# Performance work log

Measured on AMD Instinct MI355X. Metric: run time of the kernel, lower is better.

Reference implementation:

```python
import jax, jax.numpy as jnp
import numpy as np

TEXT_DIM = 1024
FEAT_DIM = 1024
NUM_HEADS = 16
HEAD_DIM = FEAT_DIM // NUM_HEADS
EPS = 1e-6


def rms_norm(x, w):
    # LlamaRMSNorm: compute in fp32, scale by learned weight
    xf = x.astype(jnp.float32)
    var = jnp.mean(xf * xf, axis=-1, keepdims=True)
    return (xf * jax.lax.rsqrt(var + EPS)).astype(x.dtype) * w


def setup_inputs() -> dict:
    key = jax.random.key(0)
    ks = jax.random.split(key, 8)
    def xavier(k, shape, gain=1.0):
        fan_in, fan_out = shape[1], shape[0]
        lim = gain * np.sqrt(6.0 / (fan_in + fan_out))
        return jax.random.uniform(k, shape, jnp.float32, -lim, lim)
    return {
        "text": jax.random.normal(ks[0], (8, 512, TEXT_DIM), jnp.float32),
        "features": jax.random.normal(ks[1], (8, 1024, FEAT_DIM), jnp.float32),
        "W_q": xavier(ks[2], (FEAT_DIM, TEXT_DIM)),
        "b_q": jnp.zeros((FEAT_DIM,), jnp.float32),
        "W_k": xavier(ks[3], (FEAT_DIM, FEAT_DIM)),
        "b_k": jnp.zeros((FEAT_DIM,), jnp.float32),
        "W_o": xavier(ks[4], (FEAT_DIM, FEAT_DIM), gain=0.1),
        "b_o": jnp.zeros((FEAT_DIM,), jnp.float32),
        "g_feat": jnp.ones((FEAT_DIM,), jnp.float32),
        "g_q": jnp.ones((FEAT_DIM,), jnp.float32),
        "g_k": jnp.ones((FEAT_DIM,), jnp.float32),
    }


def reference(text, features, W_q, b_q, W_k, b_k, W_o, b_o, g_feat, g_q, g_k):
    B, T, _ = text.shape
    _, N, _ = features.shape
    feats = rms_norm(features, g_feat)                      # [B,N,Df]
    Q = rms_norm(text @ W_q.T + b_q, g_q)                   # [B,T,Df]
    K = rms_norm(feats @ W_k.T + b_k, g_k)                  # [B,N,Df]
    Qh = Q.reshape(B, T, NUM_HEADS, HEAD_DIM)
    Kh = K.reshape(B, N, NUM_HEADS, HEAD_DIM)
    Vh = feats.reshape(B, N, NUM_HEADS, HEAD_DIM)
    scores = jnp.einsum("bthd,bnhd->bhtn", Qh, Kh) / np.sqrt(HEAD_DIM).astype(np.float32)
    attn = jax.nn.softmax(scores, axis=-1)                  # [B,H,T,N]
    out = jnp.einsum("bhtn,bnhd->bthd", attn, Vh).reshape(B, T, FEAT_DIM)
    return out @ W_o.T + b_o
```

## Files before the change

### kernel.cpp

```cpp
#include <hip/hip_runtime.h>
#include <hip/hip_bf16.h>


typedef unsigned short u16;
typedef __bf16 bf16x8 __attribute__((ext_vector_type(8)));
typedef float f32x4 __attribute__((ext_vector_type(4)));

__device__ inline f32x4 mfma16(bf16x8 a, bf16x8 b, f32x4 c) {
    return __builtin_amdgcn_mfma_f32_16x16x32_bf16(a, b, c, 0, 0, 0);
}

__device__ inline u16 f2bf(float f) {
    union { float f; unsigned u; } v; v.f = f;
    unsigned r = v.u + 0x7fffu + ((v.u >> 16) & 1u);
    return (u16)(r >> 16);
}

__device__ inline float bf2f(u16 x) {
    union { unsigned u; float f; } v; v.u = ((unsigned)x) << 16; return v.f;
}

__device__ inline unsigned pk_bf16(float a, float b) {
    union { float f; unsigned u; } x, y; x.f = a; y.f = b;
    return __builtin_amdgcn_perm(y.u + 0x8000u, x.u + 0x8000u, 0x07060302u);
}

__device__ inline void load_lds16(const void* g, void* l) {
    __builtin_amdgcn_global_load_lds(
        (const __attribute__((address_space(1))) void*)g,
        (__attribute__((address_space(3))) void*)l, 16, 0, 0);
}

__global__ __launch_bounds__(256) void cast_rows_kernel(const float* __restrict__ text,
                                                        const float* __restrict__ Wq,
                                                        const float* __restrict__ Wk,
                                                        const float* __restrict__ Wo,
                                                        const float* __restrict__ features,
                                                        u16* __restrict__ otext, u16* __restrict__ oWq,
                                                        u16* __restrict__ oWk, u16* __restrict__ oWo,
                                                        float* __restrict__ ssbuf) {
    int blk = blockIdx.x, tid = threadIdx.x;
    if (blk < 7168) {
        int i = blk * 256 + tid;
        const float* src; u16* dst; int off;
        if (i < 1048576)      { src = text; dst = otext; off = i; }
        else if (i < 1310720) { src = Wq;   dst = oWq;   off = i - 1048576; }
        else if (i < 1572864) { src = Wk;   dst = oWk;   off = i - 1310720; }
        else                  { src = Wo;   dst = oWo;   off = i - 1572864; }
        float4 v = ((const float4*)src)[off];
        uint2 p; p.x = pk_bf16(v.x, v.y); p.y = pk_bf16(v.z, v.w);
        ((uint2*)dst)[off] = p;
    } else {
        int row = (blk - 7168) * 4 + (tid >> 6);
        int lane = tid & 63;
        const float4* rp = (const float4*)(features + (size_t)row * 1024) + lane * 4;
        float ss = 0.0f;
        #pragma unroll
        for (int i = 0; i < 4; ++i) {
            float4 v = rp[i];
            ss += v.x * v.x + v.y * v.y + v.z * v.z + v.w * v.w;
        }
        #pragma unroll
        for (int m = 1; m < 64; m <<= 1) ss += __shfl_xor(ss, m, 64);
        if (lane == 0) ssbuf[row] = ss;
    }
}

__global__ __launch_bounds__(256) void normT_kernel(const float* __restrict__ features,
                                                    const float* __restrict__ ssbuf,
                                                    const float* __restrict__ g,
                                                    u16* __restrict__ feats_bf,
                                                    u16* __restrict__ Vt) {
    __shared__ __align__(16) u16 tile[64][72];
    int tid = threadIdx.x, b = blockIdx.z;
    int n0 = blockIdx.x * 64, d0 = blockIdx.y * 64;
    int r = tid >> 2, cs = (tid & 3) * 16;
    int grow = b * 1024 + n0 + r;

    float rs = rsqrtf(ssbuf[grow] * (1.0f / 1024.0f) + 1e-6f);
    const float4* src = (const float4*)(features + (size_t)grow * 1024 + d0 + cs);
    const float4* gp  = (const float4*)(g + d0 + cs);
    union { u16 s[16]; uint4 v[2]; } ob;
    #pragma unroll
    for (int i = 0; i < 4; ++i) {
        float4 v = src[i], gv = gp[i];
        unsigned lo = pk_bf16(v.x * rs * gv.x, v.y * rs * gv.y);
        unsigned hi = pk_bf16(v.z * rs * gv.z, v.w * rs * gv.w);
        ((unsigned*)ob.s)[i * 2]     = lo;
        ((unsigned*)ob.s)[i * 2 + 1] = hi;
    }
    uint4* dst = (uint4*)(feats_bf + (size_t)grow * 1024 + d0 + cs);
    dst[0] = ob.v[0]; dst[1] = ob.v[1];
    #pragma unroll
    for (int i = 0; i < 16; ++i) tile[r][cs + i] = ob.s[i];
    __syncthreads();
    union { u16 s[8]; uint4 v; } t0, t1;
    #pragma unroll
    for (int i = 0; i < 8; ++i) { t0.s[i] = tile[cs + i][r]; t1.s[i] = tile[cs + 8 + i][r]; }
    u16* tdst = Vt + ((size_t)(b * 1024 + d0 + r)) * 1024 + n0 + cs;
    *(uint4*)tdst = t0.v;
    *(uint4*)(tdst + 8) = t1.v;
}

__global__ __launch_bounds__(256) void rmsnorm_qk_kernel(u16* __restrict__ QK,
                                                         const float* __restrict__ g_q,
                                                         const float* __restrict__ g_k,
                                                         float qscale) {
    int tid = threadIdx.x;
    int row = blockIdx.x * 4 + (tid >> 6);
    int lane = tid & 63;
    const float* g = (row < 4096) ? g_q : g_k;
    float outsc = (row < 4096) ? qscale : 1.0f;

    u16* rp = QK + (size_t)row * 1024 + lane * 16;
    union { u16 s[16]; uint4 v[2]; } in;
    in.v[0] = *(const uint4*)rp;
    in.v[1] = *(const uint4*)(rp + 8);
    float x[16], ss = 0.0f;
    #pragma unroll
    for (int i = 0; i < 16; ++i) { x[i] = bf2f(in.s[i]); ss += x[i] * x[i]; }
    #pragma unroll
    for (int m = 1; m < 64; m <<= 1) ss += __shfl_xor(ss, m, 64);
    float rs = rsqrtf(ss * (1.0f / 1024.0f) + 1e-6f) * outsc;
    const float4* gp = (const float4*)(g + lane * 16);
    union { unsigned u[8]; uint4 v[2]; } ob;
    #pragma unroll
    for (int i = 0; i < 4; ++i) {
        float4 gv = gp[i];
        ob.u[i * 2]     = pk_bf16(x[i * 4 + 0] * rs * gv.x, x[i * 4 + 1] * rs * gv.y);
        ob.u[i * 2 + 1] = pk_bf16(x[i * 4 + 2] * rs * gv.z, x[i * 4 + 3] * rs * gv.w);
    }
    *(uint4*)rp = ob.v[0];
    *(uint4*)(rp + 8) = ob.v[1];
}

template <bool BF16OUT>
__device__ __forceinline__ void gemm64_bk64(const u16* __restrict__ A, const u16* __restrict__ B,
                                            const float* __restrict__ bias, void* __restrict__ Cout,
                                            int m_blk, int n_blk, int K, int N,
                                            u16* As, u16* Bs) {
    int tid = threadIdx.x, wave = tid >> 6, lane = tid & 63;
    int quad = lane >> 4, l15 = lane & 15;
    int wm = wave & 1, wn = wave >> 1;
    int arow = tid >> 2, ac = (tid & 3) * 8;

    f32x4 acc[4][2] = {};

    for (int k0 = 0; k0 < K; k0 += 64) {
        #pragma unroll
        for (int kh = 0; kh < 2; ++kh)
            #pragma unroll
            for (int rh = 0; rh < 2; ++rh)
                load_lds16(A + (size_t)(m_blk + rh * 64 + arow) * K + k0 + kh * 32 + ac,
                           As + kh * 4096 + rh * 2048 + (wave * 64) * 8);
        #pragma unroll
        for (int kh = 0; kh < 2; ++kh)
            load_lds16(B + (size_t)(n_blk + arow) * K + k0 + kh * 32 + ac,
                       Bs + kh * 2048 + (wave * 64) * 8);
        __syncthreads();
        #pragma unroll
        for (int kh = 0; kh < 2; ++kh) {
            bf16x8 af[4], bfr[2];
            #pragma unroll
            for (int t = 0; t < 4; ++t)
                af[t] = *(const bf16x8*)&As[kh * 4096 + (wm * 64 + t * 16 + l15) * 32 + quad * 8];
            #pragma unroll
            for (int t = 0; t < 2; ++t)
                bfr[t] = *(const bf16x8*)&Bs[kh * 2048 + (wn * 32 + t * 16 + l15) * 32 + quad * 8];
            #pragma unroll
            for (int mt = 0; mt < 4; ++mt)
                #pragma unroll
                for (int nt = 0; nt < 2; ++nt)
                    acc[mt][nt] = mfma16(af[mt], bfr[nt], acc[mt][nt]);
        }
        __syncthreads();
    }
    #pragma unroll
    for (int nt = 0; nt < 2; ++nt) {
        int col = n_blk + wn * 32 + nt * 16 + l15;
        float bv = bias[col];
        #pragma unroll
        for (int mt = 0; mt < 4; ++mt) {
            int row0 = m_blk + wm * 64 + mt * 16 + quad * 4;
            #pragma unroll
            for (int r = 0; r < 4; ++r) {
                float val = acc[mt][nt][r] + bv;
                if (BF16OUT) ((u16*)Cout)[(size_t)(row0 + r) * N + col] = f2bf(val);
                else       ((float*)Cout)[(size_t)(row0 + r) * N + col] = val;
            }
        }
    }
}

__global__ __launch_bounds__(256) void gemm_qk_kernel(const u16* __restrict__ text_bf,
                                                      const u16* __restrict__ Wq,
                                                      const u16* __restrict__ feats_bf,
                                                      const u16* __restrict__ Wk,
                                                      const float* __restrict__ b_q,
                                                      const float* __restrict__ b_k,
                                                      u16* __restrict__ QK) {
    __shared__ __align__(16) u16 As[2 * 128 * 32];
    __shared__ __align__(16) u16 Bs[2 * 64 * 32];
    int id = blockIdx.x;
    if (id < 512) {
        gemm64_bk64<true>(text_bf, Wq, b_q, QK, (id & 31) * 128, (id >> 5) * 64, 1024, 1024, As, Bs);
    } else {
        id -= 512;
        gemm64_bk64<true>(feats_bf, Wk, b_k, QK + 4096 * 1024,
                          (id & 63) * 128, (id >> 6) * 64, 1024, 1024, As, Bs);
    }
}

__global__ __launch_bounds__(256) void gemm_o_kernel(const u16* __restrict__ A,
                                                     const u16* __restrict__ B,
                                                     const float* __restrict__ bias,
                                                     float* __restrict__ C) {
    __shared__ __align__(16) u16 As[2 * 128 * 32];
    __shared__ __align__(16) u16 Bs[2 * 64 * 32];
    int id = blockIdx.x;
    gemm64_bk64<false>(A, B, bias, C, (id & 31) * 128, (id >> 5) * 64, 1024, 1024, As, Bs);
}

__global__ __launch_bounds__(256) void attn_kernel(const u16* __restrict__ Q,
                                                   const u16* __restrict__ K,
                                                   const u16* __restrict__ Vt,
                                                   u16* __restrict__ Out) {
    int bh = blockIdx.x, qt = blockIdx.y;
    int b = bh >> 4, h = bh & 15;
    int tid = threadIdx.x, wave = tid >> 6, lane = tid & 63;
    int quad = lane >> 4, l15 = lane & 15;

    __shared__ __align__(16) u16 Ks[64 * 64];
    __shared__ __align__(16) u16 Vs[64 * 64];
    __shared__ __align__(16) u16 Plds[4][16 * 72];
    u16* Pw = &Plds[wave][0];

    const size_t qoff = ((size_t)(b * 512 + qt * 64 + wave * 16 + l15)) * 1024 + h * 64 + quad * 8;
    bf16x8 qf0 = *(const bf16x8*)(Q + qoff);
    bf16x8 qf1 = *(const bf16x8*)(Q + qoff + 32);

    int srl = lane >> 3, scl = lane & 7;
    const u16* Kbase = K + ((size_t)(b * 1024)) * 1024 + h * 64;
    const u16* Vbase = Vt + ((size_t)(b * 1024 + h * 64)) * 1024;

    __bf16 onev = (__bf16)1.0f;
    bf16x8 ones = {onev, onev, onev, onev, onev, onev, onev, onev};

    f32x4 o[4] = {};
    f32x4 lac = {0.0f, 0.0f, 0.0f, 0.0f};

    for (int n0 = 0; n0 < 1024; n0 += 64) {
        #pragma unroll
        for (int j = 0; j < 2; ++j) {
            int row = wave * 16 + j * 8 + srl;
            load_lds16(Kbase + (size_t)(n0 + row) * 1024 + (scl ^ srl) * 8,
                       Ks + (wave * 16 + j * 8) * 64);
            load_lds16(Vbase + (size_t)row * 1024 + n0 + (scl ^ srl) * 8,
                       Vs + (wave * 16 + j * 8) * 64);
        }
        __syncthreads();

        f32x4 s[4];
        #pragma unroll
        for (int nt = 0; nt < 4; ++nt) {
            int R = nt * 16 + l15;
            int c1 = (quad ^ (l15 & 7)) * 8;
            bf16x8 kf0 = *(const bf16x8*)&Ks[R * 64 + c1];
            bf16x8 kf1 = *(const bf16x8*)&Ks[R * 64 + (c1 ^ 32)];
            f32x4 z = {-16.0f, -16.0f, -16.0f, -16.0f};
            s[nt] = mfma16(kf0, qf0, z);
            s[nt] = mfma16(kf1, qf1, s[nt]);
        }

        #pragma unroll
        for (int nt = 0; nt < 4; ++nt) {
            uint2 pk;
            pk.x = pk_bf16(exp2f(s[nt][0]), exp2f(s[nt][1]));
            pk.y = pk_bf16(exp2f(s[nt][2]), exp2f(s[nt][3]));
            *(uint2*)&Pw[l15 * 72 + nt * 16 + quad * 4] = pk;
        }

        bf16x8 pf[2];
        #pragma unroll
        for (int kc = 0; kc < 2; ++kc)
            pf[kc] = *(const bf16x8*)&Pw[l15 * 72 + kc * 32 + quad * 8];
        #pragma unroll
        for (int kc = 0; kc < 2; ++kc) {
            lac = mfma16(ones, pf[kc], lac);
            #pragma unroll
            for (int dt = 0; dt < 4; ++dt) {
                int d = dt * 16 + l15;
                int ch = ((kc * 4 + quad) ^ (l15 & 7)) * 8;
                bf16x8 vf = *(const bf16x8*)&Vs[d * 64 + ch];
                o[dt] = mfma16(vf, pf[kc], o[dt]);
            }
        }
        __syncthreads();
    }

    float il = 1.0f / lac[0];
    size_t obase = ((size_t)(b * 512 + qt * 64 + wave * 16 + l15)) * 1024 + h * 64 + quad * 4;
    #pragma unroll
    for (int dt = 0; dt < 4; ++dt) {
        uint2 pk;
        pk.x = pk_bf16(o[dt][0] * il, o[dt][1] * il);
        pk.y = pk_bf16(o[dt][2] * il, o[dt][3] * il);
        *(uint2*)(Out + obase + dt * 16) = pk;
    }
}

extern "C" void kernel_launch(void* const* d_in, const int* in_sizes, int n_in,
                              void* d_out, int out_size, void* d_ws, size_t ws_size,
                              hipStream_t stream) {
    const float* text     = (const float*)d_in[0];
    const float* features = (const float*)d_in[1];
    const float* W_q      = (const float*)d_in[2];
    const float* b_q      = (const float*)d_in[3];
    const float* W_k      = (const float*)d_in[4];
    const float* b_k      = (const float*)d_in[5];
    const float* W_o      = (const float*)d_in[6];
    const float* b_o      = (const float*)d_in[7];
    const float* g_feat   = (const float*)d_in[8];
    const float* g_q      = (const float*)d_in[9];
    const float* g_k      = (const float*)d_in[10];

    char* ws = (char*)d_ws;
    u16*   text_bf  = (u16*)(ws + 0);
    u16*   Wq_bf    = (u16*)(ws + 8388608);
    u16*   Wk_bf    = (u16*)(ws + 10485760);
    u16*   Wo_bf    = (u16*)(ws + 12582912);
    u16*   feats_bf = (u16*)(ws + 14680064);
    u16*   Vt       = (u16*)(ws + 31457280);
    u16*   QKbuf    = (u16*)(ws + 48234496);
    u16*   attn_bf  = (u16*)(ws + 73400320);
    float* ssbuf    = (float*)(ws + 81788928);

    const float QSCALE = 0.18033688011112042f;

    cast_rows_kernel<<<9216, 256, 0, stream>>>(text, W_q, W_k, W_o, features,
                                               text_bf, Wq_bf, Wk_bf, Wo_bf, ssbuf);
    normT_kernel<<<dim3(16, 16, 8), 256, 0, stream>>>(features, ssbuf, g_feat, feats_bf, Vt);
    gemm_qk_kernel<<<1536, 256, 0, stream>>>(text_bf, Wq_bf, feats_bf, Wk_bf, b_q, b_k, QKbuf);
    rmsnorm_qk_kernel<<<3072, 256, 0, stream>>>(QKbuf, g_q, g_k, QSCALE);
    attn_kernel<<<dim3(128, 8), 256, 0, stream>>>(QKbuf, QKbuf + 4096 * 1024, Vt, attn_bf);
    gemm_o_kernel<<<512, 256, 0, stream>>>(attn_bf, Wo_bf, b_o, (float*)d_out);
}
```

Measured before the change: 225.0 us.

## Split attention key range across waves with 128-key tiles and LDS reduction

The attention kernel now gives each wave a 32-key slice of a 128-key tile and all 64 query rows, instead of each wave owning 16 query rows over 64-key tiles. The partial outputs and row sums from the four waves are combined at the end through a shared-memory tree reduction. The aim is to halve the number of K/V tile loads and barriers, and to reuse each K and V fragment read from LDS across four query tiles. In exchange the kernel holds many more accumulator registers (launch bounds set to 2 blocks) and pays extra reduction and barrier cost at the end. The softmax still relies on a fixed offset instead of a running max, unchanged from before.

```diff
diff --git a/kernel.cpp b/kernel.cpp
--- a/kernel.cpp
+++ b/kernel.cpp
@@ -84,10 +84,8 @@
     #pragma unroll
     for (int i = 0; i < 4; ++i) {
         float4 v = src[i], gv = gp[i];
-        unsigned lo = pk_bf16(v.x * rs * gv.x, v.y * rs * gv.y);
-        unsigned hi = pk_bf16(v.z * rs * gv.z, v.w * rs * gv.w);
-        ((unsigned*)ob.s)[i * 2]     = lo;
-        ((unsigned*)ob.s)[i * 2 + 1] = hi;
+        ((unsigned*)ob.s)[i * 2]     = pk_bf16(v.x * rs * gv.x, v.y * rs * gv.y);
+        ((unsigned*)ob.s)[i * 2 + 1] = pk_bf16(v.z * rs * gv.z, v.w * rs * gv.w);
     }
     uint4* dst = (uint4*)(feats_bf + (size_t)grow * 1024 + d0 + cs);
     dst[0] = ob.v[0]; dst[1] = ob.v[1];
@@ -221,91 +219,148 @@
     gemm64_bk64<false>(A, B, bias, C, (id & 31) * 128, (id >> 5) * 64, 1024, 1024, As, Bs);
 }
 
-__global__ __launch_bounds__(256) void attn_kernel(const u16* __restrict__ Q,
-                                                   const u16* __restrict__ K,
-                                                   const u16* __restrict__ Vt,
-                                                   u16* __restrict__ Out) {
+__global__ __launch_bounds__(256, 2) void attn_kernel(const u16* __restrict__ Q,
+                                                      const u16* __restrict__ K,
+                                                      const u16* __restrict__ Vt,
+                                                      u16* __restrict__ Out) {
     int bh = blockIdx.x, qt = blockIdx.y;
     int b = bh >> 4, h = bh & 15;
     int tid = threadIdx.x, wave = tid >> 6, lane = tid & 63;
     int quad = lane >> 4, l15 = lane & 15;
 
-    __shared__ __align__(16) u16 Ks[64 * 64];
-    __shared__ __align__(16) u16 Vs[64 * 64];
-    __shared__ __align__(16) u16 Plds[4][16 * 72];
-    u16* Pw = &Plds[wave][0];
-
-    const size_t qoff = ((size_t)(b * 512 + qt * 64 + wave * 16 + l15)) * 1024 + h * 64 + quad * 8;
-    bf16x8 qf0 = *(const bf16x8*)(Q + qoff);
-    bf16x8 qf1 = *(const bf16x8*)(Q + qoff + 32);
-
-    int srl = lane >> 3, scl = lane & 7;
+    __shared__ __align__(16) char smem[49152];
+    u16* Ks = (u16*)smem;
+    u16* Vs = (u16*)(smem + 16384);
+    u16* Pw = (u16*)(smem + 32768) + wave * 2048;
+
+    const u16* Qbase = Q + ((size_t)(b * 512 + qt * 64)) * 1024 + h * 64;
+    bf16x8 qf[4][2];
+    #pragma unroll
+    for (int mt = 0; mt < 4; ++mt)
+        #pragma unroll
+        for (int kh = 0; kh < 2; ++kh)
+            qf[mt][kh] = *(const bf16x8*)(Qbase + (size_t)(mt * 16 + l15) * 1024 + kh * 32 + quad * 8);
+
+    int krl = lane >> 3, kcl = lane & 7;
+    int vrl = lane >> 4, vcl = lane & 15;
     const u16* Kbase = K + ((size_t)(b * 1024)) * 1024 + h * 64;
     const u16* Vbase = Vt + ((size_t)(b * 1024 + h * 64)) * 1024;
 
     __bf16 onev = (__bf16)1.0f;
     bf16x8 ones = {onev, onev, onev, onev, onev, onev, onev, onev};
 
-    f32x4 o[4] = {};
-    f32x4 lac = {0.0f, 0.0f, 0.0f, 0.0f};
-
-    for (int n0 = 0; n0 < 1024; n0 += 64) {
-        #pragma unroll
-        for (int j = 0; j < 2; ++j) {
-            int row = wave * 16 + j * 8 + srl;
-            load_lds16(Kbase + (size_t)(n0 + row) * 1024 + (scl ^ srl) * 8,
-                       Ks + (wave * 16 + j * 8) * 64);
-            load_lds16(Vbase + (size_t)row * 1024 + n0 + (scl ^ srl) * 8,
-                       Vs + (wave * 16 + j * 8) * 64);
+    f32x4 o[4][4] = {};
+    f32x4 lac[4] = {};
+
+    for (int n0 = 0; n0 < 1024; n0 += 128) {
+        #pragma unroll
+        for (int j = 0; j < 4; ++j) {
+            int krow = wave * 32 + j * 8 + krl;
+            load_lds16(Kbase + (size_t)(n0 + krow) * 1024 + (kcl ^ (krow & 7)) * 8,
+                       Ks + (wave * 32 + j * 8) * 64);
+            int vrow = wave * 16 + j * 4 + vrl;
+            load_lds16(Vbase + (size_t)vrow * 1024 + n0 + (vcl ^ (vrow & 7)) * 8,
+                       Vs + (wave * 16 + j * 4) * 128);
         }
         __syncthreads();
 
-        f32x4 s[4];
-        #pragma unroll
-        for (int nt = 0; nt < 4; ++nt) {
-            int R = nt * 16 + l15;
-            int c1 = (quad ^ (l15 & 7)) * 8;
-            bf16x8 kf0 = *(const bf16x8*)&Ks[R * 64 + c1];
-            bf16x8 kf1 = *(const bf16x8*)&Ks[R * 64 + (c1 ^ 32)];
-            f32x4 z = {-16.0f, -16.0f, -16.0f, -16.0f};
-            s[nt] = mfma16(kf0, qf0, z);
-            s[nt] = mfma16(kf1, qf1, s[nt]);
-        }
-
-        #pragma unroll
-        for (int nt = 0; nt < 4; ++nt) {
-            uint2 pk;
-            pk.x = pk_bf16(exp2f(s[nt][0]), exp2f(s[nt][1]));
-            pk.y = pk_bf16(exp2f(s[nt][2]), exp2f(s[nt][3]));
-            *(uint2*)&Pw[l15 * 72 + nt * 16 + quad * 4] = pk;
-        }
-
-        bf16x8 pf[2];
-        #pragma unroll
-        for (int kc = 0; kc < 2; ++kc)
-            pf[kc] = *(const bf16x8*)&Pw[l15 * 72 + kc * 32 + quad * 8];
-        #pragma unroll
-        for (int kc = 0; kc < 2; ++kc) {
-            lac = mfma16(ones, pf[kc], lac);
+        int ns = wave * 32;
+
+        #pragma unroll
+        for (int nt = 0; nt < 2; ++nt) {
+            int R = ns + nt * 16 + l15;
+            bf16x8 kf0 = *(const bf16x8*)&Ks[R * 64 + ((quad) ^ (l15 & 7)) * 8];
+            bf16x8 kf1 = *(const bf16x8*)&Ks[R * 64 + ((4 + quad) ^ (l15 & 7)) * 8];
+            #pragma unroll
+            for (int mt = 0; mt < 4; ++mt) {
+                f32x4 z = {-16.0f, -16.0f, -16.0f, -16.0f};
+                f32x4 s = mfma16(kf0, qf[mt][0], z);
+                s = mfma16(kf1, qf[mt][1], s);
+                uint2 pk;
+                pk.x = pk_bf16(exp2f(s[0]), exp2f(s[1]));
+                pk.y = pk_bf16(exp2f(s[2]), exp2f(s[3]));
+                int cp = (nt * 2 + (quad >> 1)) ^ (l15 & 3);
+                *(uint2*)&Pw[(mt * 16 + l15) * 32 + cp * 8 + (quad & 1) * 4] = pk;
+            }
+        }
+
+        bf16x8 pf[4];
+        #pragma unroll
+        for (int mt = 0; mt < 4; ++mt)
+            pf[mt] = *(const bf16x8*)&Pw[(mt * 16 + l15) * 32 + (quad ^ (l15 & 3)) * 8];
+        #pragma unroll
+        for (int dt = 0; dt < 4; ++dt) {
+            int d = dt * 16 + l15;
+            bf16x8 vf = *(const bf16x8*)&Vs[d * 128 + ((wave * 4 + quad) ^ (l15 & 7)) * 8];
+            #pragma unroll
+            for (int mt = 0; mt < 4; ++mt)
+                o[dt][mt] = mfma16(vf, pf[mt], o[dt][mt]);
+        }
+        #pragma unroll
+        for (int mt = 0; mt < 4; ++mt)
+            lac[mt] = mfma16(ones, pf[mt], lac[mt]);
+        __syncthreads();
+    }
+
+    float* rbuf0 = (float*)smem;
+    float* rbuf1 = (float*)(smem + 17408);
+    float* lbuf0 = (float*)(smem + 34816);
+    float* lbuf1 = (float*)(smem + 35072);
+
+    if (wave >= 2) {
+        float* rb = (wave == 2) ? rbuf0 : rbuf1;
+        float* lb = (wave == 2) ? lbuf0 : lbuf1;
+        #pragma unroll
+        for (int dt = 0; dt < 4; ++dt)
+            #pragma unroll
+            for (int mt = 0; mt < 4; ++mt)
+                *(f32x4*)&rb[(mt * 16 + l15) * 68 + dt * 16 + quad * 4] = o[dt][mt];
+        if (quad == 0)
+            #pragma unroll
+            for (int mt = 0; mt < 4; ++mt) lb[mt * 16 + l15] = lac[mt][0];
+    }
+    __syncthreads();
+    if (wave < 2) {
+        float* rb = (wave == 0) ? rbuf0 : rbuf1;
+        float* lb = (wave == 0) ? lbuf0 : lbuf1;
+        #pragma unroll
+        for (int dt = 0; dt < 4; ++dt)
+            #pragma unroll
+            for (int mt = 0; mt < 4; ++mt)
+                o[dt][mt] += *(const f32x4*)&rb[(mt * 16 + l15) * 68 + dt * 16 + quad * 4];
+        #pragma unroll
+        for (int mt = 0; mt < 4; ++mt) lac[mt][0] += lb[mt * 16 + l15];
+    }
+    __syncthreads();
+    if (wave == 1) {
+        #pragma unroll
+        for (int dt = 0; dt < 4; ++dt)
+            #pragma unroll
+            for (int mt = 0; mt < 4; ++mt)
+                *(f32x4*)&rbuf1[(mt * 16 + l15) * 68 + dt * 16 + quad * 4] = o[dt][mt];
+        if (quad == 0)
+            #pragma unroll
+            for (int mt = 0; mt < 4; ++mt) lbuf1[mt * 16 + l15] = lac[mt][0];
+    }
+    __syncthreads();
+    if (wave == 0) {
+        #pragma unroll
+        for (int dt = 0; dt < 4; ++dt)
+            #pragma unroll
+            for (int mt = 0; mt < 4; ++mt)
+                o[dt][mt] += *(const f32x4*)&rbuf1[(mt * 16 + l15) * 68 + dt * 16 + quad * 4];
+        #pragma unroll
+        for (int mt = 0; mt < 4; ++mt) {
+            float il = 1.0f / (lac[mt][0] + lbuf1[mt * 16 + l15]);
+            size_t obase = ((size_t)(b * 512 + qt * 64 + mt * 16 + l15)) * 1024 + h * 64 + quad * 4;
             #pragma unroll
             for (int dt = 0; dt < 4; ++dt) {
-                int d = dt * 16 + l15;
-                int ch = ((kc * 4 + quad) ^ (l15 & 7)) * 8;
-                bf16x8 vf = *(const bf16x8*)&Vs[d * 64 + ch];
-                o[dt] = mfma16(vf, pf[kc], o[dt]);
+                uint2 pk;
+                pk.x = pk_bf16(o[dt][mt][0] * il, o[dt][mt][1] * il);
+                pk.y = pk_bf16(o[dt][mt][2] * il, o[dt][mt][3] * il);
+                *(uint2*)(Out + obase + dt * 16) = pk;
             }
         }
-        __syncthreads();
-    }
-
-    float il = 1.0f / lac[0];
-    size_t obase = ((size_t)(b * 512 + qt * 64 + wave * 16 + l15)) * 1024 + h * 64 + quad * 4;
-    #pragma unroll
-    for (int dt = 0; dt < 4; ++dt) {
-        uint2 pk;
-        pk.x = pk_bf16(o[dt][0] * il, o[dt][1] * il);
-        pk.y = pk_bf16(o[dt][2] * il, o[dt][3] * il);
-        *(uint2*)(Out + obase + dt * 16) = pk;
     }
 }
 
```

New measurement: 234.3 us. +4.1%, slower.

## Double-buffer K/V tiles and process 32 query rows per wave in attention

Applied to the files above, without the earlier changes.

The attention kernel now handles 128 query rows per block (32 per wave, as two 16-row MFMA tiles), so each K/V tile loaded into shared memory serves twice as many queries. This halves global K/V traffic and halves the grid. K/V tiles are also double-buffered, with the next chunk's async load issued before computing the current one, removing one barrier per iteration. The cost is more registers and LDS per block and only 512 blocks, which may reduce latency hiding; launch_bounds(256,2) is added to keep occupancy.

```diff
diff --git a/kernel.cpp b/kernel.cpp
--- a/kernel.cpp
+++ b/kernel.cpp
@@ -84,10 +84,8 @@
     #pragma unroll
     for (int i = 0; i < 4; ++i) {
         float4 v = src[i], gv = gp[i];
-        unsigned lo = pk_bf16(v.x * rs * gv.x, v.y * rs * gv.y);
-        unsigned hi = pk_bf16(v.z * rs * gv.z, v.w * rs * gv.w);
-        ((unsigned*)ob.s)[i * 2]     = lo;
-        ((unsigned*)ob.s)[i * 2 + 1] = hi;
+        ((unsigned*)ob.s)[i * 2]     = pk_bf16(v.x * rs * gv.x, v.y * rs * gv.y);
+        ((unsigned*)ob.s)[i * 2 + 1] = pk_bf16(v.z * rs * gv.z, v.w * rs * gv.w);
     }
     uint4* dst = (uint4*)(feats_bf + (size_t)grow * 1024 + d0 + cs);
     dst[0] = ob.v[0]; dst[1] = ob.v[1];
@@ -221,23 +219,27 @@
     gemm64_bk64<false>(A, B, bias, C, (id & 31) * 128, (id >> 5) * 64, 1024, 1024, As, Bs);
 }
 
-__global__ __launch_bounds__(256) void attn_kernel(const u16* __restrict__ Q,
-                                                   const u16* __restrict__ K,
-                                                   const u16* __restrict__ Vt,
-                                                   u16* __restrict__ Out) {
+__global__ __launch_bounds__(256, 2) void attn_kernel(const u16* __restrict__ Q,
+                                                      const u16* __restrict__ K,
+                                                      const u16* __restrict__ Vt,
+                                                      u16* __restrict__ Out) {
     int bh = blockIdx.x, qt = blockIdx.y;
     int b = bh >> 4, h = bh & 15;
     int tid = threadIdx.x, wave = tid >> 6, lane = tid & 63;
     int quad = lane >> 4, l15 = lane & 15;
 
-    __shared__ __align__(16) u16 Ks[64 * 64];
-    __shared__ __align__(16) u16 Vs[64 * 64];
-    __shared__ __align__(16) u16 Plds[4][16 * 72];
+    __shared__ __align__(16) u16 Ksb[2][64 * 64];
+    __shared__ __align__(16) u16 Vsb[2][64 * 64];
+    __shared__ __align__(16) u16 Plds[4][32 * 72];
     u16* Pw = &Plds[wave][0];
 
-    const size_t qoff = ((size_t)(b * 512 + qt * 64 + wave * 16 + l15)) * 1024 + h * 64 + quad * 8;
-    bf16x8 qf0 = *(const bf16x8*)(Q + qoff);
-    bf16x8 qf1 = *(const bf16x8*)(Q + qoff + 32);
+    const u16* Qbase = Q + ((size_t)(b * 512 + qt * 128 + wave * 32)) * 1024 + h * 64;
+    bf16x8 qf[2][2];
+    #pragma unroll
+    for (int mt = 0; mt < 2; ++mt)
+        #pragma unroll
+        for (int kh = 0; kh < 2; ++kh)
+            qf[mt][kh] = *(const bf16x8*)(Qbase + (size_t)(mt * 16 + l15) * 1024 + kh * 32 + quad * 8);
 
     int srl = lane >> 3, scl = lane & 7;
     const u16* Kbase = K + ((size_t)(b * 1024)) * 1024 + h * 64;
@@ -246,66 +248,84 @@
     __bf16 onev = (__bf16)1.0f;
     bf16x8 ones = {onev, onev, onev, onev, onev, onev, onev, onev};
 
-    f32x4 o[4] = {};
-    f32x4 lac = {0.0f, 0.0f, 0.0f, 0.0f};
-
-    for (int n0 = 0; n0 < 1024; n0 += 64) {
-        #pragma unroll
-        for (int j = 0; j < 2; ++j) {
-            int row = wave * 16 + j * 8 + srl;
-            load_lds16(Kbase + (size_t)(n0 + row) * 1024 + (scl ^ srl) * 8,
-                       Ks + (wave * 16 + j * 8) * 64);
-            load_lds16(Vbase + (size_t)row * 1024 + n0 + (scl ^ srl) * 8,
-                       Vs + (wave * 16 + j * 8) * 64);
-        }
+    f32x4 o[4][2] = {};
+    f32x4 lac[2] = {};
+
+    #pragma unroll
+    for (int j = 0; j < 2; ++j) {
+        int row = wave * 16 + j * 8 + srl;
+        load_lds16(Kbase + (size_t)row * 1024 + (scl ^ srl) * 8, Ksb[0] + (wave * 16 + j * 8) * 64);
+        load_lds16(Vbase + (size_t)row * 1024 + (scl ^ srl) * 8, Vsb[0] + (wave * 16 + j * 8) * 64);
+    }
+
+    for (int c = 0; c < 16; ++c) {
         __syncthreads();
-
-        f32x4 s[4];
+        if (c < 15) {
+            int n1 = (c + 1) * 64;
+            #pragma unroll
+            for (int j = 0; j < 2; ++j) {
+                int row = wave * 16 + j * 8 + srl;
+                load_lds16(Kbase + (size_t)(n1 + row) * 1024 + (scl ^ srl) * 8,
+                           Ksb[(c + 1) & 1] + (wave * 16 + j * 8) * 64);
+                load_lds16(Vbase + (size_t)row * 1024 + n1 + (scl ^ srl) * 8,
+                           Vsb[(c + 1) & 1] + (wave * 16 + j * 8) * 64);
+            }
+        }
+        const u16* Ks = Ksb[c & 1];
+        const u16* Vs = Vsb[c & 1];
+
         #pragma unroll
         for (int nt = 0; nt < 4; ++nt) {
             int R = nt * 16 + l15;
             int c1 = (quad ^ (l15 & 7)) * 8;
             bf16x8 kf0 = *(const bf16x8*)&Ks[R * 64 + c1];
             bf16x8 kf1 = *(const bf16x8*)&Ks[R * 64 + (c1 ^ 32)];
-            f32x4 z = {-16.0f, -16.0f, -16.0f, -16.0f};
-            s[nt] = mfma16(kf0, qf0, z);
-            s[nt] = mfma16(kf1, qf1, s[nt]);
-        }
-
-        #pragma unroll
-        for (int nt = 0; nt < 4; ++nt) {
-            uint2 pk;
-            pk.x = pk_bf16(exp2f(s[nt][0]), exp2f(s[nt][1]));
-            pk.y = pk_bf16(exp2f(s[nt][2]), exp2f(s[nt][3]));
-            *(uint2*)&Pw[l15 * 72 + nt * 16 + quad * 4] = pk;
-        }
-
-        bf16x8 pf[2];
+            #pragma unroll
+            for (int mt = 0; mt < 2; ++mt) {
+                f32x4 z = {-16.0f, -16.0f, -16.0f, -16.0f};
+                f32x4 s = mfma16(kf0, qf[mt][0], z);
+                s = mfma16(kf1, qf[mt][1], s);
+                uint2 pk;
+                pk.x = pk_bf16(exp2f(s[0]), exp2f(s[1]));
+                pk.y = pk_bf16(exp2f(s[2]), exp2f(s[3]));
+                *(uint2*)&Pw[(mt * 16 + l15) * 72 + nt * 16 + quad * 4] = pk;
+            }
+        }
+
+        bf16x8 pf[2][2];
         #pragma unroll
         for (int kc = 0; kc < 2; ++kc)
-            pf[kc] = *(const bf16x8*)&Pw[l15 * 72 + kc * 32 + quad * 8];
+            #pragma unroll
+            for (int mt = 0; mt < 2; ++mt)
+                pf[kc][mt] = *(const bf16x8*)&Pw[(mt * 16 + l15) * 72 + kc * 32 + quad * 8];
         #pragma unroll
         for (int kc = 0; kc < 2; ++kc) {
-            lac = mfma16(ones, pf[kc], lac);
             #pragma unroll
             for (int dt = 0; dt < 4; ++dt) {
                 int d = dt * 16 + l15;
-                int ch = ((kc * 4 + quad) ^ (l15 & 7)) * 8;
-                bf16x8 vf = *(const bf16x8*)&Vs[d * 64 + ch];
-                o[dt] = mfma16(vf, pf[kc], o[dt]);
+                bf16x8 vf = *(const bf16x8*)&Vs[d * 64 + ((kc * 4 + quad) ^ (l15 & 7)) * 8];
+                #pragma unroll
+                for (int mt = 0; mt < 2; ++mt)
+                    o[dt][mt] = mfma16(vf, pf[kc][mt], o[dt][mt]);
             }
-        }
-        __syncthreads();
-    }
-
-    float il = 1.0f / lac[0];
-    size_t obase = ((size_t)(b * 512 + qt * 64 + wave * 16 + l15)) * 1024 + h * 64 + quad * 4;
-    #pragma unroll
-    for (int dt = 0; dt < 4; ++dt) {
-        uint2 pk;
-        pk.x = pk_bf16(o[dt][0] * il, o[dt][1] * il);
-        pk.y = pk_bf16(o[dt][2] * il, o[dt][3] * il);
-        *(uint2*)(Out + obase + dt * 16) = pk;
+            #pragma unroll
+            for (int mt = 0; mt < 2; ++mt)
+                lac[mt] = mfma16(ones, pf[kc][mt], lac[mt]);
+        }
+    }
+
+    #pragma unroll
+    for (int mt = 0; mt < 2; ++mt) {
+        float il = 1.0f / lac[mt][0];
+        size_t obase = ((size_t)(b * 512 + qt * 128 + wave * 32 + mt * 16 + l15)) * 1024
+                       + h * 64 + quad * 4;
+        #pragma unroll
+        for (int dt = 0; dt < 4; ++dt) {
+            uint2 pk;
+            pk.x = pk_bf16(o[dt][mt][0] * il, o[dt][mt][1] * il);
+            pk.y = pk_bf16(o[dt][mt][2] * il, o[dt][mt][3] * il);
+            *(uint2*)(Out + obase + dt * 16) = pk;
+        }
     }
 }
 
@@ -342,6 +362,6 @@
     normT_kernel<<<dim3(16, 16, 8), 256, 0, stream>>>(features, ssbuf, g_feat, feats_bf, Vt);
     gemm_qk_kernel<<<1536, 256, 0, stream>>>(text_bf, Wq_bf, feats_bf, Wk_bf, b_q, b_k, QKbuf);
     rmsnorm_qk_kernel<<<3072, 256, 0, stream>>>(QKbuf, g_q, g_k, QSCALE);
-    attn_kernel<<<dim3(128, 8), 256, 0, stream>>>(QKbuf, QKbuf + 4096 * 1024, Vt, attn_bf);
+    attn_kernel<<<dim3(128, 4), 256, 0, stream>>>(QKbuf, QKbuf + 4096 * 1024, Vt, attn_bf);
     gemm_o_kernel<<<512, 256, 0, stream>>>(attn_bf, Wo_bf, b_o, (float*)d_out);
 }
```

After: 225.7 us. No clear change (+0.3%).
